# Kernel tuning notes

Hardware: AMD Instinct MI355X
Metric: run time of the kernel (lower is better)

## Reference

```python
import jax, jax.numpy as jnp
import numpy as np

LENGTH = 14
THRESHOLD = 0.6
R = 5


def setup_inputs() -> dict:
    key = jax.random.key(0)
    B = 131072
    heatmap = jax.random.uniform(key, (B, 1, LENGTH, LENGTH), dtype=jnp.float32)
    return {"heatmap": heatmap}


def _nms_masks(heatmap):
    hm = heatmap[:, 0]  # [B,14,14]
    B = hm.shape[0]
    heat = jnp.where(hm > THRESHOLD, hm, 0.0).reshape(B, LENGTH * LENGTH)
    grid = jnp.arange(LENGTH)
    idxs = []
    # 4 rounds of argmax + zero-out-window suppression (fixed small loop)
    for _ in range(4):
        idx = jnp.argmax(heat, axis=1)  # [B]
        x = idx // LENGTH
        y = idx % LENGTH
        x1 = jnp.maximum(x - R, 0)
        y1 = jnp.maximum(y - R, 0)
        x2 = jnp.minimum(x + R, 15)  # original clamps at 15 (exclusive end)
        y2 = jnp.minimum(y + R, 15)
        rowm = (grid[None, :] >= x1[:, None]) & (grid[None, :] < x2[:, None])  # [B,14]
        colm = (grid[None, :] >= y1[:, None]) & (grid[None, :] < y2[:, None])  # [B,14]
        win = (rowm[:, :, None] & colm[:, None, :]).reshape(B, LENGTH * LENGTH)
        heat = jnp.where(win, 0.0, heat)
        idxs.append(idx)
    idxs = jnp.stack(idxs, axis=1)  # [B,4]
    coords = jnp.stack([idxs // LENGTH, idxs % LENGTH], axis=-1)  # [B,4,2]
    # pickTwo: choose the pair (among the 6) with max squared distance
    pairs = jnp.array([[0, 1], [0, 2], [0, 3], [1, 2], [1, 3], [2, 3]])
    pc = coords[:, pairs]  # [B,6,2,2]
    dists = jnp.sum((pc[:, :, 1] - pc[:, :, 0]) ** 2, axis=-1)  # [B,6]
    best = jnp.argmax(dists, axis=1)  # [B] (first max on ties, like np.argmax)
    co = jnp.take_along_axis(pc, best[:, None, None, None], axis=1)[:, 0]  # [B,2,2]
    # Voronoi-style masks: pixel belongs to mask1 iff strictly closer to co1
    u = jnp.arange(LENGTH)[:, None]  # [14,1]
    v = jnp.arange(LENGTH)[None, :]  # [1,14]
    d1 = (u[None] - co[:, 0, 0, None, None]) ** 2 + (v[None] - co[:, 0, 1, None, None]) ** 2
    d2 = (u[None] - co[:, 1, 0, None, None]) ** 2 + (v[None] - co[:, 1, 1, None, None]) ** 2
    m1 = (d1 < d2).astype(jnp.float32)  # [B,14,14]
    m2 = 1.0 - m1  # (m1 < 0.9).float() with m1 in {0,1}
    return m1[:, None], m2[:, None]  # [B,1,14,14] each


def reference(heatmap):
    return _nms_masks(heatmap)
```

## Files before the change

kernel.cpp:

```cpp
#include <hip/hip_runtime.h>


constexpr int L = 14;
constexpr int NPIX = L * L;

__global__ __launch_bounds__(256) void nms_kernel(const float* __restrict__ hm,
                                                  float* __restrict__ out,
                                                  int B) {
    const int lane = threadIdx.x & 63;
    const int b = (blockIdx.x << 2) + (threadIdx.x >> 6);
    if (b >= B) return;

    const float* __restrict__ base = hm + (size_t)b * NPIX;

    const int k0 = lane;
    const int k1 = lane + 64;
    const int k2 = lane + 128;
    const int k3 = lane + 192;
    const bool has3 = (lane < 4);

    float v0 = base[k0];
    float v1 = base[k1];
    float v2 = base[k2];
    float v3 = has3 ? base[k3] : -1.0f;

    const float TH = 0.6f;
    v0 = (v0 > TH) ? v0 : 0.0f;
    v1 = (v1 > TH) ? v1 : 0.0f;
    v2 = (v2 > TH) ? v2 : 0.0f;
    if (has3) v3 = (v3 > TH) ? v3 : 0.0f;

    const int x0 = k0 / L, y0 = k0 % L;
    const int x1e = k1 / L, y1e = k1 % L;
    const int x2e = k2 / L, y2e = k2 % L;
    const int x3e = k3 / L, y3e = k3 % L;

    int idxs[4];
#pragma unroll
    for (int r = 0; r < 4; ++r) {
        float bv = v0; int bk = k0;
        if (v1 > bv) { bv = v1; bk = k1; }
        if (v2 > bv) { bv = v2; bk = k2; }
        if (v3 > bv) { bv = v3; bk = k3; }
#pragma unroll
        for (int off = 32; off; off >>= 1) {
            float ov = __shfl_xor(bv, off, 64);
            int   ok = __shfl_xor(bk, off, 64);
            if (ov > bv || (ov == bv && ok < bk)) { bv = ov; bk = ok; }
        }
        idxs[r] = bk;
        if (r < 3) {
            const int ax = bk / L, ay = bk % L;
            const int wx1 = max(ax - 5, 0), wx2 = min(ax + 5, 15);
            const int wy1 = max(ay - 5, 0), wy2 = min(ay + 5, 15);
            if (x0  >= wx1 && x0  < wx2 && y0  >= wy1 && y0  < wy2) v0 = 0.0f;
            if (x1e >= wx1 && x1e < wx2 && y1e >= wy1 && y1e < wy2) v1 = 0.0f;
            if (x2e >= wx1 && x2e < wx2 && y2e >= wy1 && y2e < wy2) v2 = 0.0f;
            if (has3 && x3e >= wx1 && x3e < wx2 && y3e >= wy1 && y3e < wy2) v3 = 0.0f;
        }
    }

    int cx[4], cy[4];
#pragma unroll
    for (int i = 0; i < 4; ++i) { cx[i] = idxs[i] / L; cy[i] = idxs[i] % L; }

    const int pa[6] = {0, 0, 0, 1, 1, 2};
    const int pb[6] = {1, 2, 3, 2, 3, 3};
    int bestd = -1, bi = 0;
#pragma unroll
    for (int p = 0; p < 6; ++p) {
        const int dx = cx[pb[p]] - cx[pa[p]];
        const int dy = cy[pb[p]] - cy[pa[p]];
        const int d = dx * dx + dy * dy;
        if (d > bestd) { bestd = d; bi = p; }
    }
    const int ax0 = cx[pa[bi]], ay0 = cy[pa[bi]];
    const int ax1 = cx[pb[bi]], ay1 = cy[pb[bi]];

    float* __restrict__ o1 = out + (size_t)b * NPIX;
    float* __restrict__ o2 = out + (size_t)B * NPIX + (size_t)b * NPIX;

#define EMIT(X, Y, K)                                                      \
    do {                                                                   \
        const int du1 = (X) - ax0, dv1 = (Y) - ay0;                        \
        const int du2 = (X) - ax1, dv2 = (Y) - ay1;                        \
        const int d1 = du1 * du1 + dv1 * dv1;                              \
        const int d2 = du2 * du2 + dv2 * dv2;                              \
        const float m = (d1 < d2) ? 1.0f : 0.0f;                           \
        o1[(K)] = m;                                                       \
        o2[(K)] = 1.0f - m;                                                \
    } while (0)

    EMIT(x0, y0, k0);
    EMIT(x1e, y1e, k1);
    EMIT(x2e, y2e, k2);
    if (has3) EMIT(x3e, y3e, k3);
#undef EMIT
}

extern "C" void kernel_launch(void* const* d_in, const int* in_sizes, int n_in,
                              void* d_out, int out_size, void* d_ws, size_t ws_size,
                              hipStream_t stream) {
    const float* hm = (const float*)d_in[0];
    float* out = (float*)d_out;
    const int B = in_sizes[0] / NPIX;
    const int blocks = (B + 3) / 4;
    nms_kernel<<<blocks, 256, 0, stream>>>(hm, out, B);
}
```

Measured before the change: 313.9 us.

## Vectorize per-sample loads/stores as float4 and use ballot-based argmax

Each wavefront now loads its 196-pixel sample as 49 float4 values, one per lane, and writes both masks with float4 stores, replacing four scalar accesses per lane. The argmax reduction now shuffles only the max value, then uses a ballot and find-first-set to recover the lowest matching index, instead of shuffling both value and index. This cuts the number of memory instructions and shuffles. In exchange, 15 of 64 lanes sit idle during load and store, and float4 access requires each sample's base to be 16-byte aligned, which holds because 196 floats is a multiple of 4.

```diff
diff --git a/kernel.cpp b/kernel.cpp
--- a/kernel.cpp
+++ b/kernel.cpp
@@ -3,60 +3,62 @@
 
 constexpr int L = 14;
 constexpr int NPIX = L * L;
+constexpr int NV4 = NPIX / 4;
 
-__global__ __launch_bounds__(256) void nms_kernel(const float* __restrict__ hm,
-                                                  float* __restrict__ out,
+__global__ __launch_bounds__(256) void nms_kernel(const float4* __restrict__ hm4,
+                                                  float4* __restrict__ out4,
                                                   int B) {
     const int lane = threadIdx.x & 63;
     const int b = (blockIdx.x << 2) + (threadIdx.x >> 6);
     if (b >= B) return;
 
-    const float* __restrict__ base = hm + (size_t)b * NPIX;
+    const bool act = (lane < NV4);
 
-    const int k0 = lane;
-    const int k1 = lane + 64;
-    const int k2 = lane + 128;
-    const int k3 = lane + 192;
-    const bool has3 = (lane < 4);
+    float4 v4;
+    if (act) v4 = hm4[(size_t)b * NV4 + lane];
+    else     v4 = make_float4(-1.f, -1.f, -1.f, -1.f);
 
-    float v0 = base[k0];
-    float v1 = base[k1];
-    float v2 = base[k2];
-    float v3 = has3 ? base[k3] : -1.0f;
+    float va[4] = {v4.x, v4.y, v4.z, v4.w};
+    if (act) {
+#pragma unroll
+        for (int e = 0; e < 4; ++e) va[e] = (va[e] > 0.6f) ? va[e] : 0.0f;
+    }
 
-    const float TH = 0.6f;
-    v0 = (v0 > TH) ? v0 : 0.0f;
-    v1 = (v1 > TH) ? v1 : 0.0f;
-    v2 = (v2 > TH) ? v2 : 0.0f;
-    if (has3) v3 = (v3 > TH) ? v3 : 0.0f;
-
-    const int x0 = k0 / L, y0 = k0 % L;
-    const int x1e = k1 / L, y1e = k1 % L;
-    const int x2e = k2 / L, y2e = k2 % L;
-    const int x3e = k3 / L, y3e = k3 % L;
+    int xs[4], ys[4];
+#pragma unroll
+    for (int e = 0; e < 4; ++e) {
+        const int flat = 4 * lane + e;
+        xs[e] = act ? (flat / L) : 1000;
+        ys[e] = act ? (flat % L) : 1000;
+    }
 
     int idxs[4];
 #pragma unroll
     for (int r = 0; r < 4; ++r) {
-        float bv = v0; int bk = k0;
-        if (v1 > bv) { bv = v1; bk = k1; }
-        if (v2 > bv) { bv = v2; bk = k2; }
-        if (v3 > bv) { bv = v3; bk = k3; }
+        float mv = fmaxf(fmaxf(va[0], va[1]), fmaxf(va[2], va[3]));
 #pragma unroll
-        for (int off = 32; off; off >>= 1) {
-            float ov = __shfl_xor(bv, off, 64);
-            int   ok = __shfl_xor(bk, off, 64);
-            if (ov > bv || (ov == bv && ok < bk)) { bv = ov; bk = ok; }
-        }
-        idxs[r] = bk;
+        for (int off = 1; off < 64; off <<= 1)
+            mv = fmaxf(mv, __shfl_xor(mv, off, 64));
+
+        const bool h0 = (va[0] == mv), h1 = (va[1] == mv),
+                   h2 = (va[2] == mv), h3 = (va[3] == mv);
+        int e_loc = h0 ? 0 : (h1 ? 1 : (h2 ? 2 : 3));
+        const unsigned long long ball = __ballot(h0 | h1 | h2 | h3);
+        const int fl = __ffsll(ball) - 1;
+        const int e0 = __shfl(e_loc, fl, 64);
+        const int idx = 4 * fl + e0;
+        idxs[r] = idx;
+
         if (r < 3) {
-            const int ax = bk / L, ay = bk % L;
+            const int ax = idx / L, ay = idx % L;
             const int wx1 = max(ax - 5, 0), wx2 = min(ax + 5, 15);
             const int wy1 = max(ay - 5, 0), wy2 = min(ay + 5, 15);
-            if (x0  >= wx1 && x0  < wx2 && y0  >= wy1 && y0  < wy2) v0 = 0.0f;
-            if (x1e >= wx1 && x1e < wx2 && y1e >= wy1 && y1e < wy2) v1 = 0.0f;
-            if (x2e >= wx1 && x2e < wx2 && y2e >= wy1 && y2e < wy2) v2 = 0.0f;
-            if (has3 && x3e >= wx1 && x3e < wx2 && y3e >= wy1 && y3e < wy2) v3 = 0.0f;
+#pragma unroll
+            for (int e = 0; e < 4; ++e) {
+                const bool in = (xs[e] >= wx1) & (xs[e] < wx2) &
+                                (ys[e] >= wy1) & (ys[e] < wy2);
+                va[e] = in ? 0.0f : va[e];
+            }
         }
     }
 
@@ -77,33 +79,29 @@
     const int ax0 = cx[pa[bi]], ay0 = cy[pa[bi]];
     const int ax1 = cx[pb[bi]], ay1 = cy[pb[bi]];
 
-    float* __restrict__ o1 = out + (size_t)b * NPIX;
-    float* __restrict__ o2 = out + (size_t)B * NPIX + (size_t)b * NPIX;
+    float m1[4], m2[4];
+#pragma unroll
+    for (int e = 0; e < 4; ++e) {
+        const int du1 = xs[e] - ax0, dv1 = ys[e] - ay0;
+        const int du2 = xs[e] - ax1, dv2 = ys[e] - ay1;
+        const int d1 = du1 * du1 + dv1 * dv1;
+        const int d2 = du2 * du2 + dv2 * dv2;
+        m1[e] = (d1 < d2) ? 1.0f : 0.0f;
+        m2[e] = 1.0f - m1[e];
+    }
 
-#define EMIT(X, Y, K)                                                      \
-    do {                                                                   \
-        const int du1 = (X) - ax0, dv1 = (Y) - ay0;                        \
-        const int du2 = (X) - ax1, dv2 = (Y) - ay1;                        \
-        const int d1 = du1 * du1 + dv1 * dv1;                              \
-        const int d2 = du2 * du2 + dv2 * dv2;                              \
-        const float m = (d1 < d2) ? 1.0f : 0.0f;                           \
-        o1[(K)] = m;                                                       \
-        o2[(K)] = 1.0f - m;                                                \
-    } while (0)
-
-    EMIT(x0, y0, k0);
-    EMIT(x1e, y1e, k1);
-    EMIT(x2e, y2e, k2);
-    if (has3) EMIT(x3e, y3e, k3);
-#undef EMIT
+    if (act) {
+        out4[(size_t)b * NV4 + lane] = make_float4(m1[0], m1[1], m1[2], m1[3]);
+        out4[(size_t)(B + b) * NV4 + lane] = make_float4(m2[0], m2[1], m2[2], m2[3]);
+    }
 }
 
 extern "C" void kernel_launch(void* const* d_in, const int* in_sizes, int n_in,
                               void* d_out, int out_size, void* d_ws, size_t ws_size,
                               hipStream_t stream) {
-    const float* hm = (const float*)d_in[0];
-    float* out = (float*)d_out;
+    const float4* hm4 = (const float4*)d_in[0];
+    float4* out4 = (float4*)d_out;
     const int B = in_sizes[0] / NPIX;
     const int blocks = (B + 3) / 4;
-    nms_kernel<<<blocks, 256, 0, stream>>>(hm, out, B);
+    nms_kernel<<<blocks, 256, 0, stream>>>(hm4, out4, B);
 }
```

Result: faster. 296.8 us (-5.4%).
